# Performance work log

Hardware: AMD Instinct MI355X
Metric: run time of the kernel (lower is better)

Reference implementation:

```python
import jax, jax.numpy as jnp
import numpy as np

ALPHA = 0.2       # LeakyReLU negative slope
NEG_INF = -9e15   # matches torch's -9000000000000000.0 mask value


def setup_inputs() -> dict:
    key = jax.random.key(0)
    k1, k2, k3, k4, k5 = jax.random.split(key, 5)
    B, N, Fin, Fout, H = 8, 1024, 512, 512, 8
    dh = Fout // H
    return {
        "x": jax.random.normal(k1, (B, N, Fin), dtype=jnp.float32),
        "adj": jax.random.randint(k2, (B, N, N), 0, 2, dtype=jnp.int32),
        "W_w": jax.random.normal(k3, (Fin, Fout), dtype=jnp.float32) * 0.05,
        "W_b": jax.random.normal(k4, (Fout,), dtype=jnp.float32) * 0.05,
        "att": jax.random.normal(k5, (H, 2 * dh), dtype=jnp.float32) * 0.1,
    }


def reference(x, adj, W_w, W_b, att):
    # x: [B,N,Fin], adj: [B,N,N] int, W_w: [Fin,Fout], W_b: [Fout], att: [H,2*dh]
    B, N, _ = x.shape
    H = att.shape[0]
    out = x @ W_w + W_b                      # [B,N,Fout]
    dh = out.shape[-1] // H
    h = out.reshape(B, N, H, dh)             # per-head features
    a_src, a_dst = att[:, :dh], att[:, dh:]  # first half pairs with h_j, second with h_i
    s_src = jnp.einsum('bnhd,hd->bhn', h, a_src)   # contribution of source j
    s_dst = jnp.einsum('bnhd,hd->bhn', h, a_dst)   # contribution of target i
    # e[b,h,i,j] = leakyrelu(a_src . h_j + a_dst . h_i)
    e = jax.nn.leaky_relu(s_dst[:, :, :, None] + s_src[:, :, None, :], ALPHA)
    e = jnp.where(adj[:, None, :, :] > 0, e, NEG_INF)
    attn = jax.nn.softmax(e, axis=-1)              # [B,H,N,N]
    h_prime = jnp.einsum('bhij,bjhd->bihd', attn, h).reshape(B, N, H * dh)
    return jax.nn.elu(h_prime)                     # concat=True path
```

## Files before the change

kernel.cpp:

```cpp
#include <hip/hip_runtime.h>
#include <hip/hip_bf16.h>
#include <stdint.h>

typedef __attribute__((ext_vector_type(8))) short  vshort8;
typedef __attribute__((ext_vector_type(4))) float  vfloat4;
typedef __attribute__((ext_vector_type(4))) int    vint4;

static constexpr int Bb   = 8;
static constexpr int Nn   = 1024;
static constexpr int FIN  = 512;
static constexpr int FOUT = 512;
static constexpr int Hh   = 8;
static constexpr int DH   = 64;
static constexpr int Mm   = Bb * Nn;
static constexpr float LRELU_ALPHA = 0.2f;

__device__ __forceinline__ unsigned short f2bf(float f) {
  union { float f; uint32_t u; } c; c.f = f;
  uint32_t r = c.u + 0x7fffu + ((c.u >> 16) & 1u);
  return (unsigned short)(r >> 16);
}
__device__ __forceinline__ float bf2f(unsigned short s) {
  union { uint32_t u; float f; } c; c.u = ((uint32_t)s) << 16; return c.f;
}

__global__ __launch_bounds__(256) void pack_adj_kernel(const int* __restrict__ adj,
                                                       unsigned* __restrict__ pt) {
  const int gid = blockIdx.x * 256 + threadIdx.x;
  const int i = gid & 1023;
  const int w = (gid >> 10) & 31;
  const int b = gid >> 15;
  const int* src = adj + ((size_t)b * Nn + i) * Nn + w * 32;
  unsigned u = 0;
  #pragma unroll
  for (int e = 0; e < 32; ++e) u |= (src[e] > 0 ? 1u : 0u) << e;
  pt[gid] = u;
}

__global__ __launch_bounds__(256) void cast_x_kernel(const float* __restrict__ x,
                                                     short* __restrict__ xb, int n) {
  int i = (blockIdx.x * 256 + threadIdx.x) * 8;
  const int stride = gridDim.x * 256 * 8;
  for (; i < n; i += stride) {
    vfloat4 v0 = *(const vfloat4*)(x + i);
    vfloat4 v1 = *(const vfloat4*)(x + i + 4);
    vshort8 o;
    o[0] = (short)f2bf(v0[0]); o[1] = (short)f2bf(v0[1]);
    o[2] = (short)f2bf(v0[2]); o[3] = (short)f2bf(v0[3]);
    o[4] = (short)f2bf(v1[0]); o[5] = (short)f2bf(v1[1]);
    o[6] = (short)f2bf(v1[2]); o[7] = (short)f2bf(v1[3]);
    *(vshort8*)(xb + i) = o;
  }
}

__global__ __launch_bounds__(256) void transpose_w_kernel(const float* __restrict__ W,
                                                          short* __restrict__ Wt) {
  __shared__ float tile[64 * 65];
  const int n0 = blockIdx.x * 64, k0 = blockIdx.y * 64;
  const int c = threadIdx.x & 63, r4 = threadIdx.x >> 6;
  #pragma unroll
  for (int rr = 0; rr < 64; rr += 4)
    tile[(rr + r4) * 65 + c] = W[(size_t)(k0 + rr + r4) * FOUT + n0 + c];
  __syncthreads();
  #pragma unroll
  for (int rr = 0; rr < 64; rr += 4)
    Wt[(size_t)(n0 + rr + r4) * FIN + k0 + c] = (short)f2bf(tile[c * 65 + rr + r4]);
}

__global__ __launch_bounds__(256) void gemm_t_kernel(const short* __restrict__ A,
                                                     const short* __restrict__ Bt,
                                                     const float* __restrict__ bias,
                                                     short* __restrict__ hbt) {
  __shared__ short As[128 * 64];
  __shared__ short Bs[128 * 64];
  const int tid = threadIdx.x;
  const int w = tid >> 6, l = tid & 63;
  const int wv = w >> 1;
  const int wu = w & 1;
  const int lrow = l & 15, lk = l >> 4;
  const int m0 = blockIdx.x * 128, n0 = blockIdx.y * 128;
  vfloat4 acc[4][4] = {};
  for (int kt = 0; kt < FIN; kt += 64) {
    #pragma unroll
    for (int itr = 0; itr < 4; ++itr) {
      const int e = w * 2048 + itr * 512 + l * 8;
      const int row = e >> 6, col = e & 63;
      __builtin_amdgcn_global_load_lds(
          (const __attribute__((address_space(1))) unsigned int*)(A + (size_t)(m0 + row) * FIN + kt + col),
          (__attribute__((address_space(3))) unsigned int*)(As + w * 2048 + itr * 512),
          16, 0, 0);
      __builtin_amdgcn_global_load_lds(
          (const __attribute__((address_space(1))) unsigned int*)(Bt + (size_t)(n0 + row) * FIN + kt + col),
          (__attribute__((address_space(3))) unsigned int*)(Bs + w * 2048 + itr * 512),
          16, 0, 0);
    }
    __syncthreads();
    #pragma unroll
    for (int ks = 0; ks < 2; ++ks) {
      vshort8 af[4], bfr[4];
      #pragma unroll
      for (int i = 0; i < 4; ++i)
        af[i] = *(const vshort8*)(Bs + (wv * 64 + i * 16 + lrow) * 64 + ks * 32 + lk * 8);
      #pragma unroll
      for (int j = 0; j < 4; ++j)
        bfr[j] = *(const vshort8*)(As + (wu * 64 + j * 16 + lrow) * 64 + ks * 32 + lk * 8);
      #pragma unroll
      for (int i = 0; i < 4; ++i)
        #pragma unroll
        for (int j = 0; j < 4; ++j)
          acc[i][j] = __builtin_amdgcn_mfma_f32_16x16x32_bf16(af[i], bfr[j], acc[i][j], 0, 0, 0);
    }
    __syncthreads();
  }
  #pragma unroll
  for (int i = 0; i < 4; ++i) {
    const int fbase = n0 + wv * 64 + i * 16 + lk * 4;
    const vfloat4 bv = *(const vfloat4*)(bias + fbase);
    #pragma unroll
    for (int r = 0; r < 4; ++r) {
      const int fg = fbase + r;
      const int h = fg >> 6, d = fg & 63;
      #pragma unroll
      for (int j = 0; j < 4; ++j) {
        const int mg = m0 + wu * 64 + j * 16 + lrow;
        const int b = mg >> 10, n = mg & 1023;
        hbt[((size_t)(b * Hh + h) * DH + d) * Nn + n] = (short)f2bf(acc[i][j][r] + bv[r]);
      }
    }
  }
}

__global__ __launch_bounds__(256) void scores_kernel(const short* __restrict__ hbt,
                                                     const float* __restrict__ att,
                                                     float* __restrict__ ssrc,
                                                     float* __restrict__ sdst) {
  const int bh = blockIdx.y;
  const int h = bh & 7;
  const int n = blockIdx.x * 256 + threadIdx.x;
  const short* base = hbt + (size_t)bh * DH * Nn + n;
  const float* as_ = att + h * 2 * DH;
  const float* ad_ = as_ + DH;
  float ps = 0.f, pd = 0.f;
  #pragma unroll
  for (int d = 0; d < DH; ++d) {
    const float v = bf2f((unsigned short)base[(size_t)d * Nn]);
    ps += v * as_[d];
    pd += v * ad_[d];
  }
  ssrc[(size_t)bh * Nn + n] = ps;
  sdst[(size_t)bh * Nn + n] = pd;
}

__device__ __forceinline__ void stage_vb(const short* __restrict__ vbbase,
                                         short* lds_buf, int iw, int l, int jt) {
  #pragma unroll
  for (int k = 0; k < 4; ++k) {
    const int d  = iw * 16 + k * 4 + (l >> 4);
    const int cs = (l & 15) * 16;
    const int cd = cs ^ ((d & 7) << 4);
    const int j  = jt + (cd >> 1);
    __builtin_amdgcn_global_load_lds(
        (const __attribute__((address_space(1))) unsigned int*)(vbbase + (size_t)d * Nn + j),
        (__attribute__((address_space(3))) unsigned int*)(lds_buf + iw * 2048 + k * 512),
        16, 0, 0);
  }
}

__global__ __launch_bounds__(256, 4) void attn_kernel(const unsigned* __restrict__ packed,
                                                      const float* __restrict__ ssrc,
                                                      const float* __restrict__ sdst,
                                                      const short* __restrict__ hbt,
                                                      float* __restrict__ out) {
  __shared__ short vbl[2][8192];
  __shared__ float slds[1024];
  const int it = blockIdx.x, h = blockIdx.y, b = blockIdx.z;
  const int tid = threadIdx.x;
  const int iw = tid >> 6, l = tid & 63;
  const int lrow = l & 15, lk = l >> 4;
  const int i = it * 64 + iw * 16 + lrow;
  const float sdi = sdst[(size_t)(b * Hh + h) * Nn + i];
  const float* ssp = ssrc + (size_t)(b * Hh + h) * Nn;
  const short* vbbase = hbt + (size_t)(b * Hh + h) * DH * Nn;
  const unsigned* ap = packed + (size_t)b * 32 * 1024 + i;

  __builtin_amdgcn_global_load_lds(
      (const __attribute__((address_space(1))) unsigned int*)(ssp + iw * 256 + l * 4),
      (__attribute__((address_space(3))) unsigned int*)(slds + iw * 256),
      16, 0, 0);
  stage_vb(vbbase, vbl[0], iw, l, 0);
  vint4 a_cur;
  #pragma unroll
  for (int s = 0; s < 4; ++s) a_cur[s] = (int)ap[s * 1024];
  asm volatile("s_waitcnt vmcnt(0)" ::: "memory");
  asm volatile("s_barrier" ::: "memory");

  vshort8 ones;
  #pragma unroll
  for (int e = 0; e < 8; ++e) ones[e] = (short)0x3F80;
  vfloat4 acc[4] = {};
  vfloat4 accd = {};

  int buf = 0;
  for (int t = 0; t < 8; ++t) {
    vint4 a_nxt = {};
    if (t < 7) {
      stage_vb(vbbase, vbl[buf ^ 1], iw, l, (t + 1) * 128);
      #pragma unroll
      for (int s = 0; s < 4; ++s) a_nxt[s] = (int)ap[((t + 1) * 4 + s) * 1024];
      asm volatile("s_waitcnt vmcnt(8)" ::: "memory");
    } else {
      asm volatile("s_waitcnt vmcnt(0)" ::: "memory");
    }
    asm volatile("s_barrier" ::: "memory");

    const char* vc = (const char*)vbl[buf];
    const char* sc = (const char*)slds + t * 512;
    #pragma unroll
    for (int s = 0; s < 4; ++s) {
      const vfloat4 s0 = *(const vfloat4*)(sc + s * 128 + lk * 32);
      const vfloat4 s1 = *(const vfloat4*)(sc + s * 128 + lk * 32 + 16);
      const unsigned u = ((unsigned)a_cur[s]) >> (lk * 8);
      vshort8 af;
      #pragma unroll
      for (int e = 0; e < 4; ++e) {
        float tv = sdi + s0[e];
        tv = fmaxf(tv, LRELU_ALPHA * tv);
        const float pe = ((u >> e) & 1u) ? __expf(tv) : 0.f;
        af[e] = (short)__bfloat16_as_ushort(__float2bfloat16(pe));
      }
      #pragma unroll
      for (int e = 0; e < 4; ++e) {
        float tv = sdi + s1[e];
        tv = fmaxf(tv, LRELU_ALPHA * tv);
        const float pe = ((u >> (4 + e)) & 1u) ? __expf(tv) : 0.f;
        af[4 + e] = (short)__bfloat16_as_ushort(__float2bfloat16(pe));
      }
      const int cbase = (s * 64 + lk * 16) ^ ((lrow & 7) << 4);
      vshort8 f0 = *(const vshort8*)(vc + (0 * 16 + lrow) * 256 + cbase);
      vshort8 f1 = *(const vshort8*)(vc + (1 * 16 + lrow) * 256 + cbase);
      vshort8 f2 = *(const vshort8*)(vc + (2 * 16 + lrow) * 256 + cbase);
      vshort8 f3 = *(const vshort8*)(vc + (3 * 16 + lrow) * 256 + cbase);
      acc[0] = __builtin_amdgcn_mfma_f32_16x16x32_bf16(af, f0, acc[0], 0, 0, 0);
      acc[1] = __builtin_amdgcn_mfma_f32_16x16x32_bf16(af, f1, acc[1], 0, 0, 0);
      acc[2] = __builtin_amdgcn_mfma_f32_16x16x32_bf16(af, f2, acc[2], 0, 0, 0);
      acc[3] = __builtin_amdgcn_mfma_f32_16x16x32_bf16(af, f3, acc[3], 0, 0, 0);
      accd   = __builtin_amdgcn_mfma_f32_16x16x32_bf16(af, ones, accd, 0, 0, 0);
    }
    if (t < 7) a_cur = a_nxt;
    asm volatile("s_barrier" ::: "memory");
    buf ^= 1;
  }

  #pragma unroll
  for (int r = 0; r < 4; ++r) {
    const int lr = lk * 4 + r;
    const float inv = 1.0f / accd[r];
    const int row = it * 64 + iw * 16 + lr;
    #pragma unroll
    for (int df = 0; df < 4; ++df) {
      float v = acc[df][r] * inv;
      v = v > 0.f ? v : expm1f(v);
      out[((size_t)(b * Nn + row)) * FOUT + h * DH + df * 16 + lrow] = v;
    }
  }
}

extern "C" void kernel_launch(void* const* d_in, const int* in_sizes, int n_in,
                              void* d_out, int out_size, void* d_ws, size_t ws_size,
                              hipStream_t stream) {
  const float* x   = (const float*)d_in[0];
  const int*   adj = (const int*)d_in[1];
  const float* W   = (const float*)d_in[2];
  const float* Wb  = (const float*)d_in[3];
  const float* att = (const float*)d_in[4];
  float* out = (float*)d_out;

  short* xb  = (short*)d_out;
  short* Wt  = xb + (size_t)Mm * FIN;
  short* hbt = (short*)d_ws;
  float* ssrc = (float*)(hbt + (size_t)Bb * Hh * DH * Nn);
  float* sdst = ssrc + (size_t)Bb * Hh * Nn;
  unsigned* packed = (unsigned*)(sdst + (size_t)Bb * Hh * Nn);

  pack_adj_kernel<<<1024, 256, 0, stream>>>(adj, packed);
  cast_x_kernel<<<1024, 256, 0, stream>>>(x, xb, Mm * FIN);
  transpose_w_kernel<<<dim3(FOUT / 64, FIN / 64), 256, 0, stream>>>(W, Wt);
  gemm_t_kernel<<<dim3(Mm / 128, FOUT / 128), 256, 0, stream>>>(xb, Wt, Wb, hbt);
  scores_kernel<<<dim3(Nn / 256, Bb * Hh), 256, 0, stream>>>(hbt, att, ssrc, sdst);
  attn_kernel<<<dim3(Nn / 64, Hh, Bb), 256, 0, stream>>>(packed, ssrc, sdst, hbt, out);
}
```

Measured before the change: 151.0 us.

## Fuse prep kernels, shrink GEMM tiles with swizzle, vectorize scores, use exp2

Merges adjacency packing, x cast and W transpose into one launch, and rewrites adjacency packing to use wave ballots with coalesced reads. The GEMM drops to 64x64 tiles with an XOR-swizzled LDS layout, giving more blocks and fewer bank conflicts but less data reuse per block. The scores kernel now reads vectorized 8-wide chunks with an LDS reduction and folds log2(e) into the scores so the attention kernel can call the native exp2. Together these aim to cut launch overhead, uncoalesced reads and transcendental cost.

```diff
diff --git a/kernel.cpp b/kernel.cpp
--- a/kernel.cpp
+++ b/kernel.cpp
@@ -14,6 +14,7 @@
 static constexpr int DH   = 64;
 static constexpr int Mm   = Bb * Nn;
 static constexpr float LRELU_ALPHA = 0.2f;
+static constexpr float LOG2E = 1.4426950408889634f;
 
 __device__ __forceinline__ unsigned short f2bf(float f) {
   union { float f; uint32_t u; } c; c.f = f;
@@ -24,108 +25,106 @@
   union { uint32_t u; float f; } c; c.u = ((uint32_t)s) << 16; return c.f;
 }
 
-__global__ __launch_bounds__(256) void pack_adj_kernel(const int* __restrict__ adj,
-                                                       unsigned* __restrict__ pt) {
-  const int gid = blockIdx.x * 256 + threadIdx.x;
-  const int i = gid & 1023;
-  const int w = (gid >> 10) & 31;
-  const int b = gid >> 15;
-  const int* src = adj + ((size_t)b * Nn + i) * Nn + w * 32;
-  unsigned u = 0;
-  #pragma unroll
-  for (int e = 0; e < 32; ++e) u |= (src[e] > 0 ? 1u : 0u) << e;
-  pt[gid] = u;
-}
-
-__global__ __launch_bounds__(256) void cast_x_kernel(const float* __restrict__ x,
-                                                     short* __restrict__ xb, int n) {
-  int i = (blockIdx.x * 256 + threadIdx.x) * 8;
-  const int stride = gridDim.x * 256 * 8;
-  for (; i < n; i += stride) {
-    vfloat4 v0 = *(const vfloat4*)(x + i);
-    vfloat4 v1 = *(const vfloat4*)(x + i + 4);
-    vshort8 o;
-    o[0] = (short)f2bf(v0[0]); o[1] = (short)f2bf(v0[1]);
-    o[2] = (short)f2bf(v0[2]); o[3] = (short)f2bf(v0[3]);
-    o[4] = (short)f2bf(v1[0]); o[5] = (short)f2bf(v1[1]);
-    o[6] = (short)f2bf(v1[2]); o[7] = (short)f2bf(v1[3]);
-    *(vshort8*)(xb + i) = o;
-  }
-}
-
-__global__ __launch_bounds__(256) void transpose_w_kernel(const float* __restrict__ W,
-                                                          short* __restrict__ Wt) {
+__global__ __launch_bounds__(256) void prep_kernel(const int* __restrict__ adj,
+                                                   const float* __restrict__ x,
+                                                   const float* __restrict__ W,
+                                                   unsigned* __restrict__ packed,
+                                                   short* __restrict__ xb,
+                                                   short* __restrict__ Wt) {
   __shared__ float tile[64 * 65];
-  const int n0 = blockIdx.x * 64, k0 = blockIdx.y * 64;
-  const int c = threadIdx.x & 63, r4 = threadIdx.x >> 6;
-  #pragma unroll
-  for (int rr = 0; rr < 64; rr += 4)
-    tile[(rr + r4) * 65 + c] = W[(size_t)(k0 + rr + r4) * FOUT + n0 + c];
-  __syncthreads();
-  #pragma unroll
-  for (int rr = 0; rr < 64; rr += 4)
-    Wt[(size_t)(n0 + rr + r4) * FIN + k0 + c] = (short)f2bf(tile[c * 65 + rr + r4]);
+  const int bx = blockIdx.x, tid = threadIdx.x;
+  if (bx < 2048) {
+    const int rowid = bx * 4 + (tid >> 6);
+    const int b = rowid >> 10, i = rowid & 1023;
+    const int l = tid & 63;
+    const int* src = adj + (size_t)rowid * Nn;
+    unsigned myw = 0;
+    #pragma unroll
+    for (int k = 0; k < 16; ++k) {
+      const int v = src[k * 64 + l];
+      const unsigned long long m = __ballot(v > 0);
+      if (l == 2 * k)     myw = (unsigned)m;
+      if (l == 2 * k + 1) myw = (unsigned)(m >> 32);
+    }
+    if (l < 32) packed[((size_t)b * 32 + l) * 1024 + i] = myw;
+  } else if (bx < 3072) {
+    int i = ((bx - 2048) * 256 + tid) * 8;
+    const int stride = 1024 * 256 * 8;
+    for (; i < Mm * FIN; i += stride) {
+      vfloat4 v0 = *(const vfloat4*)(x + i);
+      vfloat4 v1 = *(const vfloat4*)(x + i + 4);
+      vshort8 o;
+      o[0] = (short)f2bf(v0[0]); o[1] = (short)f2bf(v0[1]);
+      o[2] = (short)f2bf(v0[2]); o[3] = (short)f2bf(v0[3]);
+      o[4] = (short)f2bf(v1[0]); o[5] = (short)f2bf(v1[1]);
+      o[6] = (short)f2bf(v1[2]); o[7] = (short)f2bf(v1[3]);
+      *(vshort8*)(xb + i) = o;
+    }
+  } else {
+    const int bxx = bx - 3072;
+    const int n0 = (bxx & 7) * 64, k0 = (bxx >> 3) * 64;
+    const int c = tid & 63, r4 = tid >> 6;
+    #pragma unroll
+    for (int rr = 0; rr < 64; rr += 4)
+      tile[(rr + r4) * 65 + c] = W[(size_t)(k0 + rr + r4) * FOUT + n0 + c];
+    __syncthreads();
+    #pragma unroll
+    for (int rr = 0; rr < 64; rr += 4)
+      Wt[(size_t)(n0 + rr + r4) * FIN + k0 + c] = (short)f2bf(tile[c * 65 + rr + r4]);
+  }
 }
 
 __global__ __launch_bounds__(256) void gemm_t_kernel(const short* __restrict__ A,
                                                      const short* __restrict__ Bt,
                                                      const float* __restrict__ bias,
                                                      short* __restrict__ hbt) {
-  __shared__ short As[128 * 64];
-  __shared__ short Bs[128 * 64];
+  __shared__ short As[64 * 64];
+  __shared__ short Bs[64 * 64];
   const int tid = threadIdx.x;
   const int w = tid >> 6, l = tid & 63;
-  const int wv = w >> 1;
-  const int wu = w & 1;
   const int lrow = l & 15, lk = l >> 4;
-  const int m0 = blockIdx.x * 128, n0 = blockIdx.y * 128;
-  vfloat4 acc[4][4] = {};
+  const int m0 = blockIdx.x * 64, n0 = blockIdx.y * 64;
+  vfloat4 acc[4] = {};
   for (int kt = 0; kt < FIN; kt += 64) {
     #pragma unroll
-    for (int itr = 0; itr < 4; ++itr) {
-      const int e = w * 2048 + itr * 512 + l * 8;
-      const int row = e >> 6, col = e & 63;
+    for (int p = 0; p < 2; ++p) {
+      const int idxS = p * 2048 + tid * 8;
+      const int row  = idxS >> 6;
+      const int cs   = (idxS & 63) * 2;
+      const int cd   = cs ^ ((row & 7) << 4);
       __builtin_amdgcn_global_load_lds(
-          (const __attribute__((address_space(1))) unsigned int*)(A + (size_t)(m0 + row) * FIN + kt + col),
-          (__attribute__((address_space(3))) unsigned int*)(As + w * 2048 + itr * 512),
-          16, 0, 0);
+          (const __attribute__((address_space(1))) unsigned int*)(A + (size_t)(m0 + row) * FIN + kt + (cd >> 1)),
+          (__attribute__((address_space(3))) unsigned int*)(As + idxS), 16, 0, 0);
       __builtin_amdgcn_global_load_lds(
-          (const __attribute__((address_space(1))) unsigned int*)(Bt + (size_t)(n0 + row) * FIN + kt + col),
-          (__attribute__((address_space(3))) unsigned int*)(Bs + w * 2048 + itr * 512),
-          16, 0, 0);
+          (const __attribute__((address_space(1))) unsigned int*)(Bt + (size_t)(n0 + row) * FIN + kt + (cd >> 1)),
+          (__attribute__((address_space(3))) unsigned int*)(Bs + idxS), 16, 0, 0);
     }
     __syncthreads();
     #pragma unroll
     for (int ks = 0; ks < 2; ++ks) {
-      vshort8 af[4], bfr[4];
-      #pragma unroll
-      for (int i = 0; i < 4; ++i)
-        af[i] = *(const vshort8*)(Bs + (wv * 64 + i * 16 + lrow) * 64 + ks * 32 + lk * 8);
-      #pragma unroll
-      for (int j = 0; j < 4; ++j)
-        bfr[j] = *(const vshort8*)(As + (wu * 64 + j * 16 + lrow) * 64 + ks * 32 + lk * 8);
-      #pragma unroll
-      for (int i = 0; i < 4; ++i)
-        #pragma unroll
-        for (int j = 0; j < 4; ++j)
-          acc[i][j] = __builtin_amdgcn_mfma_f32_16x16x32_bf16(af[i], bfr[j], acc[i][j], 0, 0, 0);
+      const int mrow = w * 16 + lrow;
+      const int gc   = ks * 64 + lk * 16;
+      vshort8 bf = *(const vshort8*)((const char*)As + mrow * 128 + (gc ^ ((mrow & 7) << 4)));
+      #pragma unroll
+      for (int i = 0; i < 4; ++i) {
+        const int frow = i * 16 + lrow;
+        vshort8 af = *(const vshort8*)((const char*)Bs + frow * 128 + (gc ^ ((frow & 7) << 4)));
+        acc[i] = __builtin_amdgcn_mfma_f32_16x16x32_bf16(af, bf, acc[i], 0, 0, 0);
+      }
     }
     __syncthreads();
   }
   #pragma unroll
   for (int i = 0; i < 4; ++i) {
-    const int fbase = n0 + wv * 64 + i * 16 + lk * 4;
+    const int fbase = n0 + i * 16 + lk * 4;
     const vfloat4 bv = *(const vfloat4*)(bias + fbase);
     #pragma unroll
     for (int r = 0; r < 4; ++r) {
       const int fg = fbase + r;
       const int h = fg >> 6, d = fg & 63;
-      #pragma unroll
-      for (int j = 0; j < 4; ++j) {
-        const int mg = m0 + wu * 64 + j * 16 + lrow;
-        const int b = mg >> 10, n = mg & 1023;
-        hbt[((size_t)(b * Hh + h) * DH + d) * Nn + n] = (short)f2bf(acc[i][j][r] + bv[r]);
-      }
+      const int mg = m0 + w * 16 + lrow;
+      const int b = mg >> 10, n = mg & 1023;
+      hbt[((size_t)(b * Hh + h) * DH + d) * Nn + n] = (short)f2bf(acc[i][r] + bv[r]);
     }
   }
 }
@@ -134,21 +133,52 @@
                                                      const float* __restrict__ att,
                                                      float* __restrict__ ssrc,
                                                      float* __restrict__ sdst) {
-  const int bh = blockIdx.y;
-  const int h = bh & 7;
-  const int n = blockIdx.x * 256 + threadIdx.x;
-  const short* base = hbt + (size_t)bh * DH * Nn + n;
-  const float* as_ = att + h * 2 * DH;
-  const float* ad_ = as_ + DH;
-  float ps = 0.f, pd = 0.f;
-  #pragma unroll
-  for (int d = 0; d < DH; ++d) {
-    const float v = bf2f((unsigned short)base[(size_t)d * Nn]);
-    ps += v * as_[d];
-    pd += v * ad_[d];
-  }
-  ssrc[(size_t)bh * Nn + n] = ps;
-  sdst[(size_t)bh * Nn + n] = pd;
+  __shared__ float lps[8][32][8];
+  __shared__ float lpd[8][32][8];
+  const int bh = blockIdx.y, h = bh & 7;
+  const int tid = threadIdx.x;
+  const int tn = tid & 31, td = tid >> 5;
+  const int n0 = blockIdx.x * 256 + tn * 8;
+  const short* base = hbt + (size_t)bh * DH * Nn;
+  float ps[8] = {}, pd[8] = {};
+  #pragma unroll
+  for (int dd = 0; dd < 8; ++dd) {
+    const int d = td * 8 + dd;
+    const vshort8 v = *(const vshort8*)(base + (size_t)d * Nn + n0);
+    const float as_ = att[h * 2 * DH + d];
+    const float ad_ = att[h * 2 * DH + DH + d];
+    #pragma unroll
+    for (int e = 0; e < 8; ++e) {
+      const float f = bf2f((unsigned short)v[e]);
+      ps[e] += f * as_;
+      pd[e] += f * ad_;
+    }
+  }
+  #pragma unroll
+  for (int e = 0; e < 8; ++e) { lps[td][tn][e] = ps[e]; lpd[td][tn][e] = pd[e]; }
+  __syncthreads();
+  if (tid < 32) {
+    float s[8] = {};
+    #pragma unroll
+    for (int q = 0; q < 8; ++q)
+      #pragma unroll
+      for (int e = 0; e < 8; ++e) s[e] += lps[q][tid][e];
+    #pragma unroll
+    for (int e = 0; e < 8; ++e) s[e] *= LOG2E;
+    *(vfloat4*)(ssrc + (size_t)bh * Nn + blockIdx.x * 256 + tid * 8) = *(vfloat4*)s;
+    *(vfloat4*)(ssrc + (size_t)bh * Nn + blockIdx.x * 256 + tid * 8 + 4) = *(vfloat4*)(s + 4);
+  } else if (tid < 64) {
+    const int t = tid - 32;
+    float s[8] = {};
+    #pragma unroll
+    for (int q = 0; q < 8; ++q)
+      #pragma unroll
+      for (int e = 0; e < 8; ++e) s[e] += lpd[q][t][e];
+    #pragma unroll
+    for (int e = 0; e < 8; ++e) s[e] *= LOG2E;
+    *(vfloat4*)(sdst + (size_t)bh * Nn + blockIdx.x * 256 + t * 8) = *(vfloat4*)s;
+    *(vfloat4*)(sdst + (size_t)bh * Nn + blockIdx.x * 256 + t * 8 + 4) = *(vfloat4*)(s + 4);
+  }
 }
 
 __device__ __forceinline__ void stage_vb(const short* __restrict__ vbbase,
@@ -225,14 +255,14 @@
       for (int e = 0; e < 4; ++e) {
         float tv = sdi + s0[e];
         tv = fmaxf(tv, LRELU_ALPHA * tv);
-        const float pe = ((u >> e) & 1u) ? __expf(tv) : 0.f;
+        const float pe = ((u >> e) & 1u) ? __builtin_amdgcn_exp2f(tv) : 0.f;
         af[e] = (short)__bfloat16_as_ushort(__float2bfloat16(pe));
       }
       #pragma unroll
       for (int e = 0; e < 4; ++e) {
         float tv = sdi + s1[e];
         tv = fmaxf(tv, LRELU_ALPHA * tv);
-        const float pe = ((u >> (4 + e)) & 1u) ? __expf(tv) : 0.f;
+        const float pe = ((u >> (4 + e)) & 1u) ? __builtin_amdgcn_exp2f(tv) : 0.f;
         af[4 + e] = (short)__bfloat16_as_ushort(__float2bfloat16(pe));
       }
       const int cbase = (s * 64 + lk * 16) ^ ((lrow & 7) << 4);
@@ -282,10 +312,8 @@
   float* sdst = ssrc + (size_t)Bb * Hh * Nn;
   unsigned* packed = (unsigned*)(sdst + (size_t)Bb * Hh * Nn);
 
-  pack_adj_kernel<<<1024, 256, 0, stream>>>(adj, packed);
-  cast_x_kernel<<<1024, 256, 0, stream>>>(x, xb, Mm * FIN);
-  transpose_w_kernel<<<dim3(FOUT / 64, FIN / 64), 256, 0, stream>>>(W, Wt);
-  gemm_t_kernel<<<dim3(Mm / 128, FOUT / 128), 256, 0, stream>>>(xb, Wt, Wb, hbt);
-  scores_kernel<<<dim3(Nn / 256, Bb * Hh), 256, 0, stream>>>(hbt, att, ssrc, sdst);
+  prep_kernel<<<3136, 256, 0, stream>>>(adj, x, W, packed, xb, Wt);
+  gemm_t_kernel<<<dim3(Mm / 64, FOUT / 64), 256, 0, stream>>>(xb, Wt, Wb, hbt);
+  scores_kernel<<<dim3(4, Bb * Hh), 256, 0, stream>>>(hbt, att, ssrc, sdst);
   attn_kernel<<<dim3(Nn / 64, Hh, Bb), 256, 0, stream>>>(packed, ssrc, sdst, hbt, out);
 }
```

New measurement: 139.4 us. 1.08x faster.
